# Optimization experiments

Hardware: AMD Instinct MI355X
Metric: run time of the kernel (lower is better)

The kernel has to match this reference:

```python
import jax, jax.numpy as jnp
import numpy as np

# B users, S candidates, H history length, T title words, D word dim, F filters, Q query dim, W window
B, S, H, T, D, F, Q, W = 64, 5, 50, 30, 300, 400, 200, 3


def _encoder_params(key, tag):
    ks = jax.random.split(key, 3)
    return {
        f"{tag}_conv_w": jax.random.normal(ks[0], (W, D, F), jnp.float32) * 0.02,
        f"{tag}_conv_b": jnp.zeros((F,), jnp.float32),
        f"{tag}_att_W": jax.random.normal(ks[1], (F, Q), jnp.float32) * 0.02,
        f"{tag}_att_b": jnp.zeros((Q,), jnp.float32),
        f"{tag}_att_q": jax.random.normal(ks[2], (Q,), jnp.float32) * 0.02,
        f"{tag}_ln_g": jnp.ones((F,), jnp.float32),
        f"{tag}_ln_b": jnp.zeros((F,), jnp.float32),
    }


def setup_inputs() -> dict:
    key = jax.random.key(0)
    k = jax.random.split(key, 8)
    inp = {
        "candidate_emb": jax.random.normal(k[0], (B, S, T, D), jnp.float32),
        "clicked_emb": jax.random.normal(k[1], (B, H, T, D), jnp.float32),
        "clicked_len": jax.random.randint(k[2], (B,), 1, H + 1),  # valid lengths >= 1
    }
    inp.update(_encoder_params(k[3], "c"))
    inp.update(_encoder_params(k[4], "u"))
    s = 1.0 / np.sqrt(F).astype(np.float32)
    inp["gru_wih"] = jax.random.uniform(k[5], (3 * F, F), jnp.float32, -s, s)
    inp["gru_whh"] = jax.random.uniform(k[6], (3 * F, F), jnp.float32, -s, s)
    inp["gru_bih"] = jnp.zeros((3 * F,), jnp.float32)
    inp["gru_bhh"] = jnp.zeros((3 * F,), jnp.float32)
    return inp


def _encode(x, conv_w, conv_b, att_W, att_b, att_q, ln_g, ln_b):
    # x: [N, T, D] -> [N, F].  Conv1d(SAME)+ReLU, additive attention pooling, LayerNorm.
    # (dropout layers are identity in eval mode)
    h = jax.lax.conv_general_dilated(
        x, conv_w, (1,), "SAME", dimension_numbers=("NWC", "WIO", "NWC")) + conv_b
    h = jax.nn.relu(h)                                                 # [N, T, F]
    a = jax.nn.softmax(jnp.tanh(h @ att_W + att_b) @ att_q, axis=1)    # [N, T]
    rep = jnp.einsum("nt,ntf->nf", a, h)                               # [N, F]
    mu = rep.mean(-1, keepdims=True)
    var = ((rep - mu) ** 2).mean(-1, keepdims=True)
    return (rep - mu) * jax.lax.rsqrt(var + 1e-5) * ln_g + ln_b


def _gru_last(x, lengths, wih, whh, bih, bhh):
    # x: [B, H, F]. Batched GRU; returns hidden state at step lengths-1 per row
    # (equivalent to pack_padded_sequence + nn.GRU last_hidden).
    def step(h, inp):
        xt, t = inp                      # xt: [B, F]
        gi = xt @ wih.T + bih            # [B, 3F]
        gh = h @ whh.T + bhh
        ir, iz, inn = jnp.split(gi, 3, axis=-1)
        hr, hz, hn = jnp.split(gh, 3, axis=-1)
        r = jax.nn.sigmoid(ir + hr)
        z = jax.nn.sigmoid(iz + hz)
        n = jnp.tanh(inn + r * hn)
        h_new = (1.0 - z) * n + z * h
        h = jnp.where((t < lengths)[:, None], h_new, h)  # freeze past each row's length
        return h, None

    h0 = jnp.zeros((x.shape[0], x.shape[2]), x.dtype)
    hT, _ = jax.lax.scan(step, h0, (x.transpose(1, 0, 2), jnp.arange(x.shape[1])))
    return hT


def reference(candidate_emb, clicked_emb, clicked_len,
              c_conv_w, c_conv_b, c_att_W, c_att_b, c_att_q, c_ln_g, c_ln_b,
              u_conv_w, u_conv_b, u_att_W, u_att_b, u_att_q, u_ln_g, u_ln_b,
              gru_wih, gru_whh, gru_bih, gru_bhh):
    # Candidate news: encode all B*S titles in one fused batch (replaces sample_num loop)
    new_rep = _encode(candidate_emb.reshape(B * S, T, D),
                      c_conv_w, c_conv_b, c_att_W, c_att_b, c_att_q,
                      c_ln_g, c_ln_b).reshape(B, S, F)
    # Clicked news: encode all B*H titles in one batch (replaces per-user loop)
    clicked_rep = _encode(clicked_emb.reshape(B * H, T, D),
                          u_conv_w, u_conv_b, u_att_W, u_att_b, u_att_q,
                          u_ln_g, u_ln_b).reshape(B, H, F)
    user_rep = _gru_last(clicked_rep, clicked_len, gru_wih, gru_whh, gru_bih, gru_bhh)  # [B, F]
    return jnp.einsum("bsf,bf->bs", new_rep, user_rep)  # score: [B, S]
```

## Files before the change

### kernel.cpp

```cpp
#include <hip/hip_runtime.h>
#include <hip/hip_bf16.h>
#include <math.h>

#define Bq 64
#define Sq 5
#define Hq 50
#define Tq 30
#define Dq 300
#define Fq 400
#define Qq 200
#define G3 1200
#define NCAND (Bq*Sq)
#define NCLK  (Bq*Hq)

typedef __attribute__((ext_vector_type(8))) short bf16x8;
typedef __attribute__((ext_vector_type(8))) _Float16 f16x8;
typedef __attribute__((ext_vector_type(4))) float f32x4;

__device__ __forceinline__ float sigmoidf_(float x){ return 1.f/(1.f+expf(-x)); }
__device__ __forceinline__ unsigned short f2bf(float x){
  __hip_bfloat16 b = __float2bfloat16(x);
  return *reinterpret_cast<unsigned short*>(&b);
}
__device__ __forceinline__ float bf2f(unsigned short u){
  __hip_bfloat16 b; *reinterpret_cast<unsigned short*>(&b) = u;
  return __bfloat162float(b);
}
typedef __attribute__((address_space(1))) const unsigned g_u32;
typedef __attribute__((address_space(3))) unsigned l_u32;
__device__ __forceinline__ void glds16(const void* g, void* l){
  __builtin_amdgcn_global_load_lds((g_u32*)g, (l_u32*)l, 16, 0, 0);
}
__device__ __forceinline__ int dot4i8(unsigned a, unsigned b, int c){
#if defined(__has_builtin) && __has_builtin(__builtin_amdgcn_sdot4)
  return __builtin_amdgcn_sdot4((int)a, (int)b, c, false);
#else
  int r = c;
  r += (int)(signed char)(a)      * (int)(signed char)(b);
  r += (int)(signed char)(a>>8)   * (int)(signed char)(b>>8);
  r += (int)(signed char)(a>>16)  * (int)(signed char)(b>>16);
  r += (int)(signed char)(a>>24)  * (int)(signed char)(b>>24);
  return r;
#endif
}

__global__ __launch_bounds__(256) void conv_prep_kernel(
    const float* __restrict__ c_cw, const float* __restrict__ u_cw,
    __hip_bfloat16* __restrict__ out)
{
  const int PER = 30*16384;
  int idx = blockIdx.x*256 + threadIdx.x;
  if (idx >= 2*PER) return;
  int enc = idx / PER, rem = idx - enc*PER;
  int chunk = rem >> 14;
  int e = rem & 16383;
  int sub = e >> 12;
  int col = (e >> 3) & 511;
  int j = e & 7;
  int w = chunk / 10, s = chunk - w*10;
  int d = s*32 + sub*8 + j;
  const float* cw = enc ? u_cw : c_cw;
  float v = (d < Dq && col < Fq) ? cw[(w*Dq + d)*Fq + col] : 0.f;
  out[idx] = __float2bfloat16(v);
}

__global__ __launch_bounds__(256) void att_prep_kernel(
    const float* __restrict__ c_aW, const float* __restrict__ u_aW,
    __hip_bfloat16* __restrict__ out)
{
  const int PER = 13*8192;
  int idx = blockIdx.x*256 + threadIdx.x;
  if (idx >= 2*PER) return;
  int enc = idx / PER, rem = idx - enc*PER;
  int chunk = rem >> 13;
  int e = rem & 8191;
  int sub = e >> 11;
  int col = (e >> 3) & 255;
  int j = e & 7;
  int k = chunk*32 + sub*8 + j;
  const float* aW = enc ? u_aW : c_aW;
  float v = (k < Fq && col < Qq) ? aW[k*Qq + col] : 0.f;
  out[idx] = __float2bfloat16(v);
}

__global__ __launch_bounds__(64) void whh_i8_prep_kernel(
    const float* __restrict__ whh, signed char* __restrict__ w8, float* __restrict__ wsc)
{
  const int g = blockIdx.x;
  const int lane = threadIdx.x;
  const float* row = whh + (size_t)g*Fq;
  float mx = 0.f;
  for (int k = lane; k < Fq; k += 64) mx = fmaxf(mx, fabsf(row[k]));
  #pragma unroll
  for (int off = 32; off >= 1; off >>= 1) mx = fmaxf(mx, __shfl_xor(mx, off));
  float inv = (mx > 0.f) ? 127.f/mx : 0.f;
  if (lane == 0) wsc[g] = mx * (1.f/16129.f);
  for (int k = lane; k < Fq; k += 64) {
    int q = (int)rintf(row[k]*inv);
    q = max(-127, min(127, q));
    w8[((size_t)(k >> 4)*G3 + g)*16 + (k & 15)] = (signed char)q;
  }
}

__global__ __launch_bounds__(256) void wihT_prep_kernel(
    const float* __restrict__ wih, _Float16* __restrict__ out)
{
  const int TOT = 13*4*G3*8;
  int idx = blockIdx.x*256 + threadIdx.x;
  if (idx >= TOT) return;
  int j = idx & 7;
  int g = (idx >> 3) % G3;
  int q = (idx >> 3) / G3;
  int sub = q & 3, s = q >> 2;
  int k = s*32 + sub*8 + j;
  out[idx] = (k < Fq) ? (_Float16)wih[(size_t)g*Fq + k] : (_Float16)0.f;
}

#define XROWS 137
#define XBYTES (40*XROWS*16)
#define BBUF0 XBYTES
#define BCHUNK 32768
#define BBUF1 (BBUF0 + BCHUNK)
#define ABUF0 (52*128*16)
#define ACHUNK 16384
#define ABUF1 (ABUF0 + ACHUNK)
#define SCRATCH (BBUF1 + BCHUNK)
#define SMEM_BYTES (SCRATCH + 1088)

__global__ __launch_bounds__(512, 2) void encode_mfma_kernel(
    const float* __restrict__ cand_emb, const float* __restrict__ clk_emb,
    const __hip_bfloat16* __restrict__ convprep,
    const __hip_bfloat16* __restrict__ attprep,
    const float* __restrict__ c_cb, const float* __restrict__ c_ab, const float* __restrict__ c_aq,
    const float* __restrict__ c_lg, const float* __restrict__ c_lb,
    const float* __restrict__ u_cb, const float* __restrict__ u_ab, const float* __restrict__ u_aq,
    const float* __restrict__ u_lg, const float* __restrict__ u_lb,
    float* __restrict__ cand_rep, float* __restrict__ clicked_rep)
{
  __shared__ __align__(16) unsigned char smem[SMEM_BYTES];
  float* sscore = (float*)(smem + SCRATCH);
  float* sa_    = sscore + 128;
  float* red_   = sa_ + 128;

  const int b = blockIdx.x, tid = threadIdx.x;
  const bool cand = b < (NCAND/4);
  const int n0 = cand ? b*4 : (b - NCAND/4)*4;
  const float* x = (cand ? cand_emb : clk_emb) + (size_t)n0*Tq*Dq;
  const __hip_bfloat16* Wp = convprep + (cand ? 0 : 30*16384);
  const __hip_bfloat16* Ap = attprep  + (cand ? 0 : 13*8192);
  const float* cb = cand ? c_cb : u_cb;
  const float* ab = cand ? c_ab : u_ab;
  const float* aq = cand ? c_aq : u_aq;
  const float* lg = cand ? c_lg : u_lg;
  const float* lb = cand ? c_lb : u_lb;

  const int lane = tid & 63, wid = tid >> 6;
  const int mh = wid >> 2, nq = wid & 3;
  const int l15 = lane & 15, l4 = lane >> 4;
  const int wbase16 = (tid & ~63)*16;

  if (tid < 128) sscore[tid] = 0.f;

  #pragma unroll
  for (int k = 0; k < 4; ++k)
    glds16(Wp + k*4096 + tid*8, smem + BBUF0 + k*8192 + wbase16);

  for (int i = tid; i < 40*XROWS; i += 512) {
    int c = i % 40, r = i / 40;
    f32x4 va = (f32x4){0.f,0.f,0.f,0.f}, vb = (f32x4){0.f,0.f,0.f,0.f};
    if (r < 128) {
      int lr = r & 31, tt = r >> 5;
      if (lr >= 1 && lr <= 30) {
        int t = lr - 1, d0 = c*8;
        if (d0 < Dq) {
          const f32x4* src = (const f32x4*)(x + (size_t)tt*Tq*Dq + t*Dq + d0);
          va = __builtin_nontemporal_load(src);
          if (d0 + 4 < Dq) vb = __builtin_nontemporal_load(src + 1);
        }
      }
    }
    union { bf16x8 v; unsigned short u[8]; } pk;
    pk.u[0]=f2bf(va.x); pk.u[1]=f2bf(va.y); pk.u[2]=f2bf(va.z); pk.u[3]=f2bf(va.w);
    pk.u[4]=f2bf(vb.x); pk.u[5]=f2bf(vb.y); pk.u[6]=f2bf(vb.z); pk.u[7]=f2bf(vb.w);
    *(bf16x8*)(smem + (size_t)(c*XROWS + r)*16) = pk.v;
  }

  f32x4 acc[4][7];
  float cbv[7];
  #pragma unroll
  for (int nf = 0; nf < 7; ++nf) {
    int colg = (nq*7 + nf)*16 + l15;
    cbv[nf] = (colg < Fq) ? cb[colg] : 0.f;
  }
  #pragma unroll
  for (int mf = 0; mf < 4; ++mf)
    #pragma unroll
    for (int nf = 0; nf < 7; ++nf)
      acc[mf][nf] = (f32x4){cbv[nf], cbv[nf], cbv[nf], cbv[nf]};

  __syncthreads();

  for (int step = 0; step < 30; ++step) {
    const int w = step / 10, s = step - w*10;
    const int cbuf = step & 1;
    if (step < 29) {
      const __hip_bfloat16* src = Wp + (size_t)(step+1)*16384;
      unsigned char* dst = smem + (cbuf ? BBUF0 : BBUF1);
      #pragma unroll
      for (int k = 0; k < 4; ++k)
        glds16(src + k*4096 + tid*8, dst + k*8192 + wbase16);
    }
    bf16x8 a[4];
    #pragma unroll
    for (int mf = 0; mf < 4; ++mf) {
      int arow = mh*64 + mf*16 + l15 + w;
      int c = s*4 + l4;
      a[mf] = *(const bf16x8*)(smem + (size_t)(c*XROWS + arow)*16);
    }
    bf16x8 bb[7];
    const unsigned char* bbase = smem + (cbuf ? BBUF1 : BBUF0);
    #pragma unroll
    for (int nf = 0; nf < 7; ++nf) {
      int col = (nq*7 + nf)*16 + l15;
      bb[nf] = *(const bf16x8*)(bbase + (size_t)(l4*512 + col)*16);
    }
    #pragma unroll
    for (int mf = 0; mf < 4; ++mf)
      #pragma unroll
      for (int nf = 0; nf < 7; ++nf)
        acc[mf][nf] = __builtin_amdgcn_mfma_f32_16x16x32_bf16(a[mf], bb[nf], acc[mf][nf], 0, 0, 0);
    __syncthreads();
  }

  #pragma unroll
  for (int k = 0; k < 2; ++k)
    glds16(Ap + k*4096 + tid*8, smem + ABUF0 + k*8192 + wbase16);

  #pragma unroll
  for (int mf = 0; mf < 4; ++mf) {
    #pragma unroll
    for (int nf = 0; nf < 7; ++nf) {
      int colg = (nq*7 + nf)*16 + l15;
      if (colg < 416) {
        #pragma unroll
        for (int i = 0; i < 4; ++i) {
          int row = mh*64 + mf*16 + l4*4 + i;
          float v = fmaxf(acc[mf][nf][i], 0.f);
          *(unsigned short*)(smem + (size_t)((colg >> 3)*128 + row)*16 + (colg & 7)*2) = f2bf(v);
        }
      }
    }
  }
  __syncthreads();

  f32x4 acc2[4][4];
  #pragma unroll
  for (int mf = 0; mf < 4; ++mf)
    #pragma unroll
    for (int nn = 0; nn < 4; ++nn)
      acc2[mf][nn] = (f32x4){0.f,0.f,0.f,0.f};
  const int nf0  = (nq == 0) ? 0 : (1 + 3*nq);
  const int ncnt = (nq == 0) ? 4 : 3;

  for (int s2 = 0; s2 < 13; ++s2) {
    const int cbuf = s2 & 1;
    if (s2 < 12) {
      const __hip_bfloat16* src = Ap + (size_t)(s2+1)*8192;
      unsigned char* dst = smem + (cbuf ? ABUF0 : ABUF1);
      #pragma unroll
      for (int k = 0; k < 2; ++k)
        glds16(src + k*4096 + tid*8, dst + k*8192 + wbase16);
    }
    bf16x8 a2[4];
    #pragma unroll
    for (int mf = 0; mf < 4; ++mf) {
      int row = mh*64 + mf*16 + l15;
      int fchunk = s2*4 + l4;
      a2[mf] = *(const bf16x8*)(smem + (size_t)(fchunk*128 + row)*16);
    }
    bf16x8 b2[4];
    const unsigned char* bbase = smem + (cbuf ? ABUF1 : ABUF0);
    #pragma unroll
    for (int nn = 0; nn < 4; ++nn) {
      if (nn < ncnt) {
        int col = (nf0 + nn)*16 + l15;
        b2[nn] = *(const bf16x8*)(bbase + (size_t)(l4*256 + col)*16);
      }
    }
    #pragma unroll
    for (int mf = 0; mf < 4; ++mf)
      #pragma unroll
      for (int nn = 0; nn < 4; ++nn)
        if (nn < ncnt)
          acc2[mf][nn] = __builtin_amdgcn_mfma_f32_16x16x32_bf16(a2[mf], b2[nn], acc2[mf][nn], 0, 0, 0);
    __syncthreads();
  }

  {
    float abv[4], aqv[4];
    #pragma unroll
    for (int nn = 0; nn < 4; ++nn) {
      int col = (nf0 + nn)*16 + l15;
      bool ok = (nn < ncnt) && (col < Qq);
      abv[nn] = ok ? ab[col] : 0.f;
      aqv[nn] = ok ? aq[col] : 0.f;
    }
    #pragma unroll
    for (int mf = 0; mf < 4; ++mf) {
      #pragma unroll
      for (int i = 0; i < 4; ++i) {
        float p = 0.f;
        #pragma unroll
        for (int nn = 0; nn < 4; ++nn)
          if (nn < ncnt)
            p += tanhf(acc2[mf][nn][i] + abv[nn]) * aqv[nn];
        p += __shfl_xor(p, 1); p += __shfl_xor(p, 2);
        p += __shfl_xor(p, 4); p += __shfl_xor(p, 8);
        if (l15 == 0) atomicAdd(&sscore[mh*64 + mf*16 + l4*4 + i], p);
      }
    }
  }
  __syncthreads();

  if (tid < 4) {
    float mx = -1e30f;
    for (int t = 0; t < Tq; ++t) mx = fmaxf(mx, sscore[tid*32 + t]);
    float sum = 0.f;
    for (int t = 0; t < Tq; ++t) { float e = expf(sscore[tid*32 + t] - mx); sa_[tid*32 + t] = e; sum += e; }
    float inv = 1.f / sum;
    for (int t = 0; t < Tq; ++t) sa_[tid*32 + t] *= inv;
    sa_[tid*32 + 30] = 0.f; sa_[tid*32 + 31] = 0.f;
  }
  __syncthreads();

  {
    const int tt = tid >> 7, fb = tid & 127;
    float rv[4];
    float ls = 0.f, lsq = 0.f;
    #pragma unroll
    for (int q = 0; q < 4; ++q) {
      int f = fb + q*128;
      rv[q] = 0.f;
      if (f < Fq) {
        float r = 0.f;
        const unsigned char* hb = smem + (size_t)(f >> 3)*128*16 + (f & 7)*2;
        for (int t = 0; t < Tq; ++t)
          r += sa_[tt*32 + t] * bf2f(*(const unsigned short*)(hb + (size_t)(tt*32 + t)*16));
        rv[q] = r; ls += r; lsq += r*r;
      }
    }
    #pragma unroll
    for (int off = 32; off >= 1; off >>= 1) { ls += __shfl_xor(ls, off); lsq += __shfl_xor(lsq, off); }
    if (lane == 0) { red_[wid] = ls; red_[8 + wid] = lsq; }
    __syncthreads();
    float tot  = red_[2*tt] + red_[2*tt + 1];
    float totq = red_[8 + 2*tt] + red_[8 + 2*tt + 1];
    float mu = tot * (1.f/Fq);
    float var = totq * (1.f/Fq) - mu*mu;
    float rs = rsqrtf(var + 1e-5f);
    float* dst = (cand ? cand_rep : clicked_rep) + (size_t)(n0 + tt)*Fq;
    #pragma unroll
    for (int q = 0; q < 4; ++q) {
      int f = fb + q*128;
      if (f < Fq) dst[f] = (rv[q] - mu)*rs*lg[f] + lb[f];
    }
  }
}

__global__ __launch_bounds__(256) void gi_mfma_kernel(
    const float* __restrict__ rep, const _Float16* __restrict__ wihT,
    const float* __restrict__ bih, float* __restrict__ gi)
{
  __shared__ __align__(16) _Float16 As[2][4][64][8];
  __shared__ __align__(16) _Float16 Bs[2][4][240][8];
  const int tid = threadIdx.x;
  const int bm = blockIdx.x;
  const int nc = blockIdx.y;
  const int lane = tid & 63, wv = tid >> 6;
  const int l15 = lane & 15, l4 = lane >> 4;
  const int arow = tid >> 2, asub = tid & 3;

  f32x4 acc[15];
  #pragma unroll
  for (int nf = 0; nf < 15; ++nf) acc[nf] = (f32x4){0.f,0.f,0.f,0.f};

  auto stage = [&](int p, int s){
    {
      f32x4 v0 = (f32x4){0.f,0.f,0.f,0.f}, v1 = v0;
      int k0 = s*32 + asub*8;
      if (k0 < Fq) {
        const f32x4* src = (const f32x4*)(rep + (size_t)(bm*64 + arow)*Fq + k0);
        v0 = src[0]; v1 = src[1];
      }
      union { f16x8 v; _Float16 e[8]; } pk;
      pk.e[0]=(_Float16)v0.x; pk.e[1]=(_Float16)v0.y; pk.e[2]=(_Float16)v0.z; pk.e[3]=(_Float16)v0.w;
      pk.e[4]=(_Float16)v1.x; pk.e[5]=(_Float16)v1.y; pk.e[6]=(_Float16)v1.z; pk.e[7]=(_Float16)v1.w;
      *(f16x8*)&As[p][asub][arow][0] = pk.v;
    }
    const _Float16* bsrc = wihT + (size_t)s*4*G3*8;
    uint4* bdst = (uint4*)&Bs[p][0][0][0];
    for (int i = tid; i < 960; i += 256) {
      int sub = i / 240, col = i - sub*240;
      bdst[i] = *(const uint4*)(bsrc + ((size_t)sub*G3 + nc*240 + col)*8);
    }
  };

  stage(0, 0);
  __syncthreads();

  for (int s = 0; s < 13; ++s) {
    const int p = s & 1;
    if (s < 12) stage(p ^ 1, s + 1);
    f16x8 a = *(const f16x8*)&As[p][l4][wv*16 + l15][0];
    #pragma unroll
    for (int nf = 0; nf < 15; ++nf) {
      f16x8 bfr = *(const f16x8*)&Bs[p][l4][nf*16 + l15][0];
      acc[nf] = __builtin_amdgcn_mfma_f32_16x16x32_f16(a, bfr, acc[nf], 0, 0, 0);
    }
    __syncthreads();
  }

  #pragma unroll
  for (int nf = 0; nf < 15; ++nf) {
    int g = nc*240 + nf*16 + l15;
    float bv = bih[g];
    #pragma unroll
    for (int i = 0; i < 4; ++i) {
      int row = bm*64 + wv*16 + l4*4 + i;
      gi[(size_t)row*G3 + g] = acc[nf][i] + bv;
    }
  }
}

__global__ __launch_bounds__(1024) void gru_kernel(
    const float* __restrict__ gi, const signed char* __restrict__ w8,
    const float* __restrict__ wsc, const float* __restrict__ bhh,
    const int* __restrict__ lens, float* __restrict__ user_rep)
{
  __shared__ __align__(16) float shf[Fq];
  __shared__ __align__(16) signed char sh8[Fq];
  __shared__ float sgh[G3];
  const int b = blockIdx.x, tid = threadIdx.x;
  const int len = lens[b];
  for (int j = tid; j < Fq; j += 1024) { shf[j] = 0.f; sh8[j] = 0; }
  __syncthreads();
  const int g2 = tid + 1024;
  const bool g2ok = (g2 < G3);
  const uint4* w1 = (const uint4*)w8 + tid;
  const uint4* w2 = (const uint4*)w8 + (g2ok ? g2 : tid);
  const float sc1 = wsc[tid];
  const float sc2 = g2ok ? wsc[g2] : 0.f;
  const float bb1 = bhh[tid];
  const float bb2 = g2ok ? bhh[g2] : 0.f;
  const float* gb = gi + (size_t)b*Hq*G3;

  for (int t = 0; t < len; ++t) {
    int a1 = 0, a2 = 0;
    const uint4* hp = (const uint4*)sh8;
    #pragma unroll 5
    for (int k16 = 0; k16 < 25; ++k16) {
      uint4 hv = hp[k16];
      uint4 wv = w1[(size_t)k16*G3];
      a1 = dot4i8(hv.x, wv.x, a1); a1 = dot4i8(hv.y, wv.y, a1);
      a1 = dot4i8(hv.z, wv.z, a1); a1 = dot4i8(hv.w, wv.w, a1);
      if (g2ok) {
        uint4 vv = w2[(size_t)k16*G3];
        a2 = dot4i8(hv.x, vv.x, a2); a2 = dot4i8(hv.y, vv.y, a2);
        a2 = dot4i8(hv.z, vv.z, a2); a2 = dot4i8(hv.w, vv.w, a2);
      }
    }
    sgh[tid] = (float)a1*sc1 + bb1;
    if (g2ok) sgh[g2] = (float)a2*sc2 + bb2;
    __syncthreads();
    if (tid < Fq) {
      float gr = __builtin_nontemporal_load(&gb[tid]);
      float gz = __builtin_nontemporal_load(&gb[Fq + tid]);
      float gn = __builtin_nontemporal_load(&gb[2*Fq + tid]);
      float r  = sigmoidf_(gr + sgh[tid]);
      float z  = sigmoidf_(gz + sgh[Fq + tid]);
      float nn = tanhf   (gn + r*sgh[2*Fq + tid]);
      float hn = (1.f - z)*nn + z*shf[tid];
      shf[tid] = hn;
      int q = (int)rintf(hn*127.f);
      sh8[tid] = (signed char)max(-127, min(127, q));
    }
    __syncthreads();
    gb += G3;
  }
  for (int j = tid; j < Fq; j += 1024) user_rep[(size_t)b*Fq + j] = shf[j];
}

__global__ __launch_bounds__(64) void score_kernel(
    const float* __restrict__ cand_rep, const float* __restrict__ user_rep,
    float* __restrict__ out)
{
  const int i = blockIdx.x;
  const int b = i / Sq;
  const int lane = threadIdx.x;
  float acc = 0.f;
  for (int f = lane; f < Fq; f += 64) acc = fmaf(cand_rep[(size_t)i*Fq+f], user_rep[(size_t)b*Fq+f], acc);
  #pragma unroll
  for (int off = 32; off >= 1; off >>= 1) acc += __shfl_xor(acc, off);
  if (lane == 0) out[i] = acc;
}

extern "C" void kernel_launch(void* const* d_in, const int* in_sizes, int n_in,
                              void* d_out, int out_size, void* d_ws, size_t ws_size,
                              hipStream_t stream)
{
  const float* cand_emb = (const float*)d_in[0];
  const float* clk_emb  = (const float*)d_in[1];
  const int*   lens     = (const int*)  d_in[2];
  const float* c_cw = (const float*)d_in[3];
  const float* c_cb = (const float*)d_in[4];
  const float* c_aW = (const float*)d_in[5];
  const float* c_ab = (const float*)d_in[6];
  const float* c_aq = (const float*)d_in[7];
  const float* c_lg = (const float*)d_in[8];
  const float* c_lb = (const float*)d_in[9];
  const float* u_cw = (const float*)d_in[10];
  const float* u_cb = (const float*)d_in[11];
  const float* u_aW = (const float*)d_in[12];
  const float* u_ab = (const float*)d_in[13];
  const float* u_aq = (const float*)d_in[14];
  const float* u_lg = (const float*)d_in[15];
  const float* u_lb = (const float*)d_in[16];
  const float* wih  = (const float*)d_in[17];
  const float* whh  = (const float*)d_in[18];
  const float* bih  = (const float*)d_in[19];
  const float* bhh  = (const float*)d_in[20];

  float* ws = (float*)d_ws;
  float* cand_rep    = ws;
  float* clicked_rep = cand_rep + NCAND*Fq;
  float* gi          = clicked_rep + NCLK*Fq;
  float* user_rep    = gi + (size_t)NCLK*G3;
  signed char* w8    = (signed char*)(user_rep + Bq*Fq);
  float* wsc         = (float*)(w8 + 480000);
  _Float16* wihT16   = (_Float16*)(wsc + 1200);
  __hip_bfloat16* convprep = (__hip_bfloat16*)gi;
  __hip_bfloat16* attprep  = (__hip_bfloat16*)(gi + 491520);

  conv_prep_kernel<<<(2*30*16384 + 255)/256, 256, 0, stream>>>(c_cw, u_cw, convprep);
  att_prep_kernel<<<(2*13*8192 + 255)/256, 256, 0, stream>>>(c_aW, u_aW, attprep);
  whh_i8_prep_kernel<<<G3, 64, 0, stream>>>(whh, w8, wsc);
  wihT_prep_kernel<<<(13*4*G3*8 + 255)/256, 256, 0, stream>>>(wih, wihT16);

  encode_mfma_kernel<<<(NCAND + NCLK)/4, 512, 0, stream>>>(
      cand_emb, clk_emb, convprep, attprep,
      c_cb, c_ab, c_aq, c_lg, c_lb,
      u_cb, u_ab, u_aq, u_lg, u_lb,
      cand_rep, clicked_rep);

  gi_mfma_kernel<<<dim3(NCLK/64, 5), 256, 0, stream>>>(clicked_rep, wihT16, bih, gi);

  gru_kernel<<<Bq, 1024, 0, stream>>>(gi, w8, wsc, bhh, lens, user_rep);

  score_kernel<<<NCAND, 64, 0, stream>>>(cand_rep, user_rep, (float*)d_out);
}
```

Before: 501.1 us.

## Keep GRU recurrent int8 weights in registers and LDS, prefetch next-step gates

The GRU kernel now uses 512 threads, each holding two rows of the int8 recurrent weight matrix in registers (50 uint4), while the remaining 176 rows are staged in padded shared memory. This removes the per-timestep global/L2 reloads of the 480KB weight matrix. The input-gate values for the next timestep are also loaded before the barrier, which overlaps that latency with compute. The cost is high register pressure (200 VGPRs for weights alone) that may cause spills, plus unbalanced work across lanes for the LDS-resident rows.

New measurement: 617.5 us. +23.2%, slower.

```diff
diff --git a/kernel.cpp b/kernel.cpp
--- a/kernel.cpp
+++ b/kernel.cpp
@@ -42,6 +42,11 @@
   r += (int)(signed char)(a>>24)  * (int)(signed char)(b>>24);
   return r;
 #endif
+}
+__device__ __forceinline__ int dot16i8(uint4 h, uint4 w, int c){
+  c = dot4i8(h.x, w.x, c); c = dot4i8(h.y, w.y, c);
+  c = dot4i8(h.z, w.z, c); c = dot4i8(h.w, w.w, c);
+  return c;
 }
 
 __global__ __launch_bounds__(256) void conv_prep_kernel(
@@ -432,50 +437,72 @@
   }
 }
 
-__global__ __launch_bounds__(1024) void gru_kernel(
+__global__ __launch_bounds__(512, 2) void gru_reg_kernel(
     const float* __restrict__ gi, const signed char* __restrict__ w8,
     const float* __restrict__ wsc, const float* __restrict__ bhh,
     const int* __restrict__ lens, float* __restrict__ user_rep)
 {
-  __shared__ __align__(16) float shf[Fq];
+  __shared__ float shf[Fq];
   __shared__ __align__(16) signed char sh8[Fq];
   __shared__ float sgh[G3];
+  __shared__ unsigned cw[25*176*5];
   const int b = blockIdx.x, tid = threadIdx.x;
+  const int lane = tid & 63, wv = tid >> 6;
   const int len = lens[b];
-  for (int j = tid; j < Fq; j += 1024) { shf[j] = 0.f; sh8[j] = 0; }
+
+  uint4 wA[25], wB[25];
+  const uint4* w16 = (const uint4*)w8;
+  #pragma unroll
+  for (int i = 0; i < 25; ++i) {
+    wA[i] = w16[(size_t)i*G3 + tid];
+    wB[i] = w16[(size_t)i*G3 + 512 + tid];
+  }
+  for (int idx = tid; idx < 25*176*4; idx += 512) {
+    int i = idx / 704, r = idx - i*704;
+    int c = r >> 2, d = r & 3;
+    cw[(i*176 + c)*5 + d] = ((const unsigned*)w8)[((size_t)i*G3 + 1024 + c)*4 + d];
+  }
+  for (int j = tid; j < Fq; j += 512) shf[j] = 0.f;
+  for (int j = tid; j < 100; j += 512) ((unsigned*)sh8)[j] = 0u;
+
+  const int cid = wv*22 + (lane < 22 ? lane : 0);
+  const bool cok = (lane < 22);
+  const float sc1 = wsc[tid],     sc2 = wsc[512 + tid], sc3 = cok ? wsc[1024 + cid] : 0.f;
+  const float bb1 = bhh[tid],     bb2 = bhh[512 + tid], bb3 = cok ? bhh[1024 + cid] : 0.f;
+  const float* gb = gi + (size_t)b*Hq*G3;
+
   __syncthreads();
-  const int g2 = tid + 1024;
-  const bool g2ok = (g2 < G3);
-  const uint4* w1 = (const uint4*)w8 + tid;
-  const uint4* w2 = (const uint4*)w8 + (g2ok ? g2 : tid);
-  const float sc1 = wsc[tid];
-  const float sc2 = g2ok ? wsc[g2] : 0.f;
-  const float bb1 = bhh[tid];
-  const float bb2 = g2ok ? bhh[g2] : 0.f;
-  const float* gb = gi + (size_t)b*Hq*G3;
+
+  float gr = 0.f, gz = 0.f, gn = 0.f;
+  if (tid < Fq) { gr = gb[tid]; gz = gb[Fq + tid]; gn = gb[2*Fq + tid]; }
 
   for (int t = 0; t < len; ++t) {
-    int a1 = 0, a2 = 0;
+    int a1 = 0, a2 = 0, a3 = 0;
     const uint4* hp = (const uint4*)sh8;
-    #pragma unroll 5
-    for (int k16 = 0; k16 < 25; ++k16) {
-      uint4 hv = hp[k16];
-      uint4 wv = w1[(size_t)k16*G3];
-      a1 = dot4i8(hv.x, wv.x, a1); a1 = dot4i8(hv.y, wv.y, a1);
-      a1 = dot4i8(hv.z, wv.z, a1); a1 = dot4i8(hv.w, wv.w, a1);
-      if (g2ok) {
-        uint4 vv = w2[(size_t)k16*G3];
-        a2 = dot4i8(hv.x, vv.x, a2); a2 = dot4i8(hv.y, vv.y, a2);
-        a2 = dot4i8(hv.z, vv.z, a2); a2 = dot4i8(hv.w, vv.w, a2);
-      }
-    }
-    sgh[tid] = (float)a1*sc1 + bb1;
-    if (g2ok) sgh[g2] = (float)a2*sc2 + bb2;
+    #pragma unroll
+    for (int i = 0; i < 25; ++i) {
+      uint4 hv = hp[i];
+      a1 = dot16i8(hv, wA[i], a1);
+      a2 = dot16i8(hv, wB[i], a2);
+      if (cok) {
+        const unsigned* cp = &cw[(i*176 + cid)*5];
+        a3 = dot4i8(hv.x, cp[0], a3);
+        a3 = dot4i8(hv.y, cp[1], a3);
+        a3 = dot4i8(hv.z, cp[2], a3);
+        a3 = dot4i8(hv.w, cp[3], a3);
+      }
+    }
+    sgh[tid]       = (float)a1*sc1 + bb1;
+    sgh[512 + tid] = (float)a2*sc2 + bb2;
+    if (cok) sgh[1024 + cid] = (float)a3*sc3 + bb3;
+
+    float ngr = 0.f, ngz = 0.f, ngn = 0.f;
+    if (tid < Fq && (t + 1) < len) {
+      const float* g2p = gb + (size_t)(t + 1)*G3;
+      ngr = g2p[tid]; ngz = g2p[Fq + tid]; ngn = g2p[2*Fq + tid];
+    }
     __syncthreads();
     if (tid < Fq) {
-      float gr = __builtin_nontemporal_load(&gb[tid]);
-      float gz = __builtin_nontemporal_load(&gb[Fq + tid]);
-      float gn = __builtin_nontemporal_load(&gb[2*Fq + tid]);
       float r  = sigmoidf_(gr + sgh[tid]);
       float z  = sigmoidf_(gz + sgh[Fq + tid]);
       float nn = tanhf   (gn + r*sgh[2*Fq + tid]);
@@ -485,9 +512,9 @@
       sh8[tid] = (signed char)max(-127, min(127, q));
     }
     __syncthreads();
-    gb += G3;
-  }
-  for (int j = tid; j < Fq; j += 1024) user_rep[(size_t)b*Fq + j] = shf[j];
+    gr = ngr; gz = ngz; gn = ngn;
+  }
+  if (tid < Fq) user_rep[(size_t)b*Fq + tid] = shf[tid];
 }
 
 __global__ __launch_bounds__(64) void score_kernel(
@@ -554,7 +581,7 @@
 
   gi_mfma_kernel<<<dim3(NCLK/64, 5), 256, 0, stream>>>(clicked_rep, wihT16, bih, gi);
 
-  gru_kernel<<<Bq, 1024, 0, stream>>>(gi, w8, wsc, bhh, lens, user_rep);
+  gru_reg_kernel<<<Bq, 512, 0, stream>>>(gi, w8, wsc, bhh, lens, user_rep);
 
   score_kernel<<<NCAND, 64, 0, stream>>>(cand_rep, user_rep, (float*)d_out);
 }
```

## Halve encoder tile to two titles per 256-thread block, drop weight double buffering

Applied to the files above, without the earlier changes.

The encoder kernel now processes 2 titles per block with 4 waves instead of 4 titles with 8 waves, which doubles the grid and halves the shared-memory footprint. The conv and attention weight chunks are now single-buffered: the load of the next chunk starts after a barrier and an extra barrier follows it, so global-to-LDS loads no longer overlap the MFMA work. Input loads switch from nontemporal to regular loads. The goal is more resident blocks per CU and better occupancy. The cost is that each weight chunk is reused by half as many rows, doubling weight traffic, and the load latency is exposed on every step.

Measured after the change: 519.0 us. 1.04x slower.

```diff
diff --git a/kernel.cpp b/kernel.cpp
--- a/kernel.cpp
+++ b/kernel.cpp
@@ -15,6 +15,7 @@
 
 typedef __attribute__((ext_vector_type(8))) short bf16x8;
 typedef __attribute__((ext_vector_type(8))) _Float16 f16x8;
+typedef __attribute__((ext_vector_type(2))) _Float16 h2;
 typedef __attribute__((ext_vector_type(4))) float f32x4;
 
 __device__ __forceinline__ float sigmoidf_(float x){ return 1.f/(1.f+expf(-x)); }
@@ -116,18 +117,13 @@
   out[idx] = (k < Fq) ? (_Float16)wih[(size_t)g*Fq + k] : (_Float16)0.f;
 }
 
-#define XROWS 137
-#define XBYTES (40*XROWS*16)
-#define BBUF0 XBYTES
-#define BCHUNK 32768
-#define BBUF1 (BBUF0 + BCHUNK)
-#define ABUF0 (52*128*16)
-#define ACHUNK 16384
-#define ABUF1 (ABUF0 + ACHUNK)
-#define SCRATCH (BBUF1 + BCHUNK)
-#define SMEM_BYTES (SCRATCH + 1088)
-
-__global__ __launch_bounds__(512, 2) void encode_mfma_kernel(
+#define XR 67
+#define CBOF 42880
+#define ABOF 53248
+#define SCROF 75648
+#define SMEMB (SCROF + 576)
+
+__global__ __launch_bounds__(256, 2) void encode_mfma_kernel(
     const float* __restrict__ cand_emb, const float* __restrict__ clk_emb,
     const __hip_bfloat16* __restrict__ convprep,
     const __hip_bfloat16* __restrict__ attprep,
@@ -137,14 +133,14 @@
     const float* __restrict__ u_lg, const float* __restrict__ u_lb,
     float* __restrict__ cand_rep, float* __restrict__ clicked_rep)
 {
-  __shared__ __align__(16) unsigned char smem[SMEM_BYTES];
-  float* sscore = (float*)(smem + SCRATCH);
-  float* sa_    = sscore + 128;
-  float* red_   = sa_ + 128;
+  __shared__ __align__(16) unsigned char smem[SMEMB];
+  float* sscore = (float*)(smem + SCROF);
+  float* sa_    = sscore + 64;
+  float* red_   = sa_ + 64;
 
   const int b = blockIdx.x, tid = threadIdx.x;
-  const bool cand = b < (NCAND/4);
-  const int n0 = cand ? b*4 : (b - NCAND/4)*4;
+  const bool cand = b < (NCAND/2);
+  const int n0 = cand ? b*2 : (b - NCAND/2)*2;
   const float* x = (cand ? cand_emb : clk_emb) + (size_t)n0*Tq*Dq;
   const __hip_bfloat16* Wp = convprep + (cand ? 0 : 30*16384);
   const __hip_bfloat16* Ap = attprep  + (cand ? 0 : 13*8192);
@@ -154,75 +150,67 @@
   const float* lg = cand ? c_lg : u_lg;
   const float* lb = cand ? c_lb : u_lb;
 
-  const int lane = tid & 63, wid = tid >> 6;
-  const int mh = wid >> 2, nq = wid & 3;
+  const int lane = tid & 63, nq = tid >> 6;
   const int l15 = lane & 15, l4 = lane >> 4;
   const int wbase16 = (tid & ~63)*16;
 
-  if (tid < 128) sscore[tid] = 0.f;
-
-  #pragma unroll
-  for (int k = 0; k < 4; ++k)
-    glds16(Wp + k*4096 + tid*8, smem + BBUF0 + k*8192 + wbase16);
-
-  for (int i = tid; i < 40*XROWS; i += 512) {
+  if (tid < 64) sscore[tid] = 0.f;
+
+  #pragma unroll
+  for (int k = 0; k < 8; ++k)
+    glds16(Wp + k*2048 + tid*8, smem + CBOF + k*4096 + wbase16);
+
+  for (int i = tid; i < 40*XR; i += 256) {
     int c = i % 40, r = i / 40;
     f32x4 va = (f32x4){0.f,0.f,0.f,0.f}, vb = (f32x4){0.f,0.f,0.f,0.f};
-    if (r < 128) {
+    if (r < 64) {
       int lr = r & 31, tt = r >> 5;
       if (lr >= 1 && lr <= 30) {
         int t = lr - 1, d0 = c*8;
         if (d0 < Dq) {
           const f32x4* src = (const f32x4*)(x + (size_t)tt*Tq*Dq + t*Dq + d0);
-          va = __builtin_nontemporal_load(src);
-          if (d0 + 4 < Dq) vb = __builtin_nontemporal_load(src + 1);
+          va = src[0];
+          if (d0 + 4 < Dq) vb = src[1];
         }
       }
     }
     union { bf16x8 v; unsigned short u[8]; } pk;
     pk.u[0]=f2bf(va.x); pk.u[1]=f2bf(va.y); pk.u[2]=f2bf(va.z); pk.u[3]=f2bf(va.w);
     pk.u[4]=f2bf(vb.x); pk.u[5]=f2bf(vb.y); pk.u[6]=f2bf(vb.z); pk.u[7]=f2bf(vb.w);
-    *(bf16x8*)(smem + (size_t)(c*XROWS + r)*16) = pk.v;
+    *(bf16x8*)(smem + (size_t)(c*XR + r)*16) = pk.v;
   }
 
   f32x4 acc[4][7];
-  float cbv[7];
-  #pragma unroll
-  for (int nf = 0; nf < 7; ++nf) {
-    int colg = (nq*7 + nf)*16 + l15;
-    cbv[nf] = (colg < Fq) ? cb[colg] : 0.f;
-  }
-  #pragma unroll
-  for (int mf = 0; mf < 4; ++mf)
-    #pragma unroll
-    for (int nf = 0; nf < 7; ++nf)
-      acc[mf][nf] = (f32x4){cbv[nf], cbv[nf], cbv[nf], cbv[nf]};
+  {
+    float cbv[7];
+    #pragma unroll
+    for (int nf = 0; nf < 7; ++nf) {
+      int colg = (nq*7 + nf)*16 + l15;
+      cbv[nf] = (colg < Fq) ? cb[colg] : 0.f;
+    }
+    #pragma unroll
+    for (int mf = 0; mf < 4; ++mf)
+      #pragma unroll
+      for (int nf = 0; nf < 7; ++nf)
+        acc[mf][nf] = (f32x4){cbv[nf], cbv[nf], cbv[nf], cbv[nf]};
+  }
 
   __syncthreads();
 
   for (int step = 0; step < 30; ++step) {
     const int w = step / 10, s = step - w*10;
-    const int cbuf = step & 1;
-    if (step < 29) {
-      const __hip_bfloat16* src = Wp + (size_t)(step+1)*16384;
-      unsigned char* dst = smem + (cbuf ? BBUF0 : BBUF1);
-      #pragma unroll
-      for (int k = 0; k < 4; ++k)
-        glds16(src + k*4096 + tid*8, dst + k*8192 + wbase16);
-    }
     bf16x8 a[4];
     #pragma unroll
     for (int mf = 0; mf < 4; ++mf) {
-      int arow = mh*64 + mf*16 + l15 + w;
+      int arow = mf*16 + l15 + w;
       int c = s*4 + l4;
-      a[mf] = *(const bf16x8*)(smem + (size_t)(c*XROWS + arow)*16);
+      a[mf] = *(const bf16x8*)(smem + (size_t)(c*XR + arow)*16);
     }
     bf16x8 bb[7];
-    const unsigned char* bbase = smem + (cbuf ? BBUF1 : BBUF0);
     #pragma unroll
     for (int nf = 0; nf < 7; ++nf) {
       int col = (nq*7 + nf)*16 + l15;
-      bb[nf] = *(const bf16x8*)(bbase + (size_t)(l4*512 + col)*16);
+      bb[nf] = *(const bf16x8*)(smem + CBOF + (size_t)(l4*512 + col)*16);
     }
     #pragma unroll
     for (int mf = 0; mf < 4; ++mf)
@@ -230,12 +218,18 @@
       for (int nf = 0; nf < 7; ++nf)
         acc[mf][nf] = __builtin_amdgcn_mfma_f32_16x16x32_bf16(a[mf], bb[nf], acc[mf][nf], 0, 0, 0);
     __syncthreads();
-  }
-
-  #pragma unroll
-  for (int k = 0; k < 2; ++k)
-    glds16(Ap + k*4096 + tid*8, smem + ABUF0 + k*8192 + wbase16);
-
+    if (step < 29) {
+      const __hip_bfloat16* src = Wp + (size_t)(step+1)*16384;
+      #pragma unroll
+      for (int k = 0; k < 8; ++k)
+        glds16(src + k*2048 + tid*8, smem + CBOF + k*4096 + wbase16);
+    }
+    __syncthreads();
+  }
+
+  #pragma unroll
+  for (int k = 0; k < 4; ++k)
+    glds16(Ap + k*2048 + tid*8, smem + ABOF + k*4096 + wbase16);
   #pragma unroll
   for (int mf = 0; mf < 4; ++mf) {
     #pragma unroll
@@ -244,9 +238,9 @@
       if (colg < 416) {
         #pragma unroll
         for (int i = 0; i < 4; ++i) {
-          int row = mh*64 + mf*16 + l4*4 + i;
+          int row = mf*16 + l4*4 + i;
           float v = fmaxf(acc[mf][nf][i], 0.f);
-          *(unsigned short*)(smem + (size_t)((colg >> 3)*128 + row)*16 + (colg & 7)*2) = f2bf(v);
+          *(unsigned short*)(smem + (size_t)((colg >> 3)*64 + row)*16 + (colg & 7)*2) = f2bf(v);
         }
       }
     }
@@ -263,28 +257,19 @@
   const int ncnt = (nq == 0) ? 4 : 3;
 
   for (int s2 = 0; s2 < 13; ++s2) {
-    const int cbuf = s2 & 1;
-    if (s2 < 12) {
-      const __hip_bfloat16* src = Ap + (size_t)(s2+1)*8192;
-      unsigned char* dst = smem + (cbuf ? ABUF0 : ABUF1);
-      #pragma unroll
-      for (int k = 0; k < 2; ++k)
-        glds16(src + k*4096 + tid*8, dst + k*8192 + wbase16);
-    }
     bf16x8 a2[4];
     #pragma unroll
     for (int mf = 0; mf < 4; ++mf) {
-      int row = mh*64 + mf*16 + l15;
+      int row = mf*16 + l15;
       int fchunk = s2*4 + l4;
-      a2[mf] = *(const bf16x8*)(smem + (size_t)(fchunk*128 + row)*16);
+      a2[mf] = *(const bf16x8*)(smem + (size_t)(fchunk*64 + row)*16);
     }
     bf16x8 b2[4];
-    const unsigned char* bbase = smem + (cbuf ? ABUF1 : ABUF0);
     #pragma unroll
     for (int nn = 0; nn < 4; ++nn) {
       if (nn < ncnt) {
         int col = (nf0 + nn)*16 + l15;
-        b2[nn] = *(const bf16x8*)(bbase + (size_t)(l4*256 + col)*16);
+        b2[nn] = *(const bf16x8*)(smem + ABOF + (size_t)(l4*256 + col)*16);
       }
     }
     #pragma unroll
@@ -293,6 +278,13 @@
       for (int nn = 0; nn < 4; ++nn)
         if (nn < ncnt)
           acc2[mf][nn] = __builtin_amdgcn_mfma_f32_16x16x32_bf16(a2[mf], b2[nn], acc2[mf][nn], 0, 0, 0);
+    __syncthreads();
+    if (s2 < 12) {
+      const __hip_bfloat16* src = Ap + (size_t)(s2+1)*8192;
+      #pragma unroll
+      for (int k = 0; k < 4; ++k)
+        glds16(src + k*2048 + tid*8, smem + ABOF + k*4096 + wbase16);
+    }
     __syncthreads();
   }
 
@@ -316,13 +308,13 @@
             p += tanhf(acc2[mf][nn][i] + abv[nn]) * aqv[nn];
         p += __shfl_xor(p, 1); p += __shfl_xor(p, 2);
         p += __shfl_xor(p, 4); p += __shfl_xor(p, 8);
-        if (l15 == 0) atomicAdd(&sscore[mh*64 + mf*16 + l4*4 + i], p);
+        if (l15 == 0) atomicAdd(&sscore[mf*16 + l4*4 + i], p);
       }
     }
   }
   __syncthreads();
 
-  if (tid < 4) {
+  if (tid < 2) {
     float mx = -1e30f;
     for (int t = 0; t < Tq; ++t) mx = fmaxf(mx, sscore[tid*32 + t]);
     float sum = 0.f;
@@ -343,18 +335,19 @@
       rv[q] = 0.f;
       if (f < Fq) {
         float r = 0.f;
-        const unsigned char* hb = smem + (size_t)(f >> 3)*128*16 + (f & 7)*2;
+        const unsigned char* hb = smem + (size_t)(f >> 3)*64*16 + (f & 7)*2;
         for (int t = 0; t < Tq; ++t)
           r += sa_[tt*32 + t] * bf2f(*(const unsigned short*)(hb + (size_t)(tt*32 + t)*16));
         rv[q] = r; ls += r; lsq += r*r;
       }
     }
+    const int wid = tid >> 6;
     #pragma unroll
     for (int off = 32; off >= 1; off >>= 1) { ls += __shfl_xor(ls, off); lsq += __shfl_xor(lsq, off); }
-    if (lane == 0) { red_[wid] = ls; red_[8 + wid] = lsq; }
+    if (lane == 0) { red_[wid] = ls; red_[4 + wid] = lsq; }
     __syncthreads();
     float tot  = red_[2*tt] + red_[2*tt + 1];
-    float totq = red_[8 + 2*tt] + red_[8 + 2*tt + 1];
+    float totq = red_[4 + 2*tt] + red_[4 + 2*tt + 1];
     float mu = tot * (1.f/Fq);
     float var = totq * (1.f/Fq) - mu*mu;
     float rs = rsqrtf(var + 1e-5f);
@@ -546,7 +539,7 @@
   whh_i8_prep_kernel<<<G3, 64, 0, stream>>>(whh, w8, wsc);
   wihT_prep_kernel<<<(13*4*G3*8 + 255)/256, 256, 0, stream>>>(wih, wihT16);
 
-  encode_mfma_kernel<<<(NCAND + NCLK)/4, 512, 0, stream>>>(
+  encode_mfma_kernel<<<(NCAND + NCLK)/2, 256, 0, stream>>>(
       cand_emb, clk_emb, convprep, attprep,
       c_cb, c_ab, c_aq, c_lg, c_lb,
       u_cb, u_ab, u_aq, u_lg, u_lb,
```
